# Optimization experiments

Measured on AMD Instinct MI355X. Metric: run time of the kernel, lower is better.

Reference implementation:

```python
import jax, jax.numpy as jnp
import numpy as np

N = 768          # nodes
E_HALF = 12288   # undirected edges (both directions added -> E = 24576)
P = 4096         # query pairs
H = 32           # hidden_dim_1wl == hidden_dim_2wl
MAX_X = 100
EPS = 1e-5
LAYER1 = 2


def setup_inputs() -> dict:
    key = jax.random.key(0)
    ks = jax.random.split(key, 12)
    s = 0.1
    x = jax.random.randint(ks[0], (N,), 0, MAX_X + 1)
    half = jax.random.randint(ks[1], (2, E_HALF), 0, N)
    ei = jnp.concatenate([half, half[::-1]], axis=1)          # symmetric edge set [2,E]
    pos = jax.random.randint(ks[2], (P, 2), 0, N)
    emb = jax.random.normal(ks[3], (MAX_X + 1, H)) * s
    gcn_W = jax.random.normal(ks[4], (LAYER1, H, H)) * s
    gcn_b = jnp.zeros((LAYER1, H))
    mlp1_W = jax.random.normal(ks[5], (2 * H, H)) * s
    mlp1_b = jnp.zeros((H,))
    mlp2_W = jax.random.normal(ks[6], (2 * H, H)) * s
    mlp2_b = jnp.zeros((H,))
    mlp3_W = jax.random.normal(ks[7], (H + 1, H)) * s
    mlp3_b = jnp.zeros((H,))
    lin_W = jax.random.normal(ks[8], (2 * H, 1)) * s
    lin_b = jnp.zeros((1,))
    return dict(x=x, ei=ei, pos=pos, emb=emb, gcn_W=gcn_W, gcn_b=gcn_b,
                mlp1_W=mlp1_W, mlp1_b=mlp1_b, mlp2_W=mlp2_W, mlp2_b=mlp2_b,
                mlp3_W=mlp3_W, mlp3_b=mlp3_b, lin_W=lin_W, lin_b=lin_b)


def _graph_norm(h):
    # PyG-style GraphNorm with default params (mean_scale=1, weight=1, bias=0)
    h = h - h.mean(0)
    return h * jax.lax.rsqrt((h * h).mean(0) + EPS)


def reference(x, ei, pos, emb, gcn_W, gcn_b, mlp1_W, mlp1_b,
              mlp2_W, mlp2_b, mlp3_W, mlp3_b, lin_W, lin_b):
    n = x.shape[0]
    d = emb.shape[1]
    h = emb[x]                                                 # [n,H] (dropout=0)
    # --- GCNConv stack: Ahat = D^-1/2 (A+I) D^-1/2 ---
    A = jnp.zeros((n, n), h.dtype).at[ei[0], ei[1]].set(1.0)
    Ahat = A + jnp.eye(n, dtype=h.dtype)
    dinv = jax.lax.rsqrt(Ahat.sum(1))
    An = Ahat * dinv[:, None] * dinv[None, :]
    for l in range(gcn_W.shape[0]):
        h = An @ (h @ gcn_W[l]) + gcn_b[l]
        h = jax.nn.relu(_graph_norm(h))                        # GraphNorm + ReLU
    # --- pair features ---
    xx = h[pos[:, 0]] * h[pos[:, 1]]                           # [P,H]
    val = jnp.concatenate([h[ei[0]], h[ei[1]]], 1)             # [E,2H]
    xe = jax.nn.relu(val @ mlp1_W + mlp1_b)                    # mlps_1
    mul = jax.nn.relu(val @ mlp2_W + mlp2_b)                   # mlps_2[0]
    # --- sparse_bmm as dense [n,n,d] contraction (coalesce sums duplicates -> .add) ---
    Xd = jnp.zeros((n, n, d), h.dtype).at[ei[0], ei[1]].add(xe)
    Md = jnp.zeros((n, n, d), h.dtype).at[ei[0], ei[1]].add(mul)
    C = jnp.einsum('ikd,kjd->ijd', Xd, Md)                     # x_{ij} = sum_k x_{ik}*mul_{kj}
    # support of the sparse result: 2-hop pairs union original edges (sparse_cat)
    adj_b = jnp.zeros((n, n), bool).at[ei[0], ei[1]].set(True)
    af = adj_b.astype(h.dtype)
    mask = ((af @ af) > 0) | adj_b
    ind = af[..., None]                                        # ones-column for original edges
    value = jnp.concatenate([C, ind], -1)                      # [n,n,H+1]
    z = value @ mlp3_W + mlp3_b                                # mlps_3[0]
    # GraphNorm over the edge support only (faithful to sparse values())
    m = mask.astype(h.dtype)[..., None]
    cnt = m.sum()
    mean = (z * m).sum((0, 1)) / cnt
    z = z - mean
    var = ((z * z) * m).sum((0, 1)) / cnt
    z = jax.nn.relu(z * jax.lax.rsqrt(var + EPS))
    # x * sm: multiply by transposed values; zero outside support (= add_zero)
    sym = z * jnp.swapaxes(z, 0, 1) * m
    pair = sym[pos[:, 0], pos[:, 1]]                           # [P,H] (edge_list gather)
    out = jnp.concatenate([pair, xx], 1) @ lin_W + lin_b       # lin_dir -> [P,1]
    return out
```

## Files before the change

kernel.cpp:

```cpp
#include <hip/hip_runtime.h>
#include <hip/hip_bf16.h>

#define NN 768
#define NE 24576
#define NPOS 4096
#define NCELL (NN*NN)
#define NBLK 2304
#define NBLK2 1152
#define NREP 16

typedef __hip_bfloat16 bf16;

__device__ __forceinline__ float ldf(const void* p, int i, int mode) {
    return mode ? __bfloat162float(((const bf16*)p)[i]) : ((const float*)p)[i];
}
__device__ __forceinline__ float aread(float* p) { return atomicAdd(p, 0.f); }
__device__ __forceinline__ int areadi(int* p) { return atomicAdd(p, 0); }

template<int D, int HALF>
__device__ __forceinline__ void redRound(float* v, int lane) {
#pragma unroll
    for (int i = 0; i < HALF; i++) {
        float snd = (lane & D) ? v[i] : v[i + HALF];
        float r = __shfl_xor(snd, D);
        v[i] = ((lane & D) ? v[i + HALF] : v[i]) + r;
    }
}

#define DOT4(Z, A, W) Z += A.x * W.x + A.y * W.y + A.z * W.z + A.w * W.w

#define GATH(rec, q0,q1,q2,q3,q4,q5,q6,q7) { \
    const float4* xr = xep4 + (rec).x * 8; \
    const float4* mr = mulp4 + (rec).y * 8; \
    float4 xv0 = xr[0], xv1 = xr[1], xv2 = xr[2], xv3 = xr[3]; \
    float4 xv4 = xr[4], xv5 = xr[5], xv6 = xr[6], xv7 = xr[7]; \
    float4 mv0 = mr[0], mv1 = mr[1], mv2 = mr[2], mv3 = mr[3]; \
    float4 mv4 = mr[4], mv5 = mr[5], mv6 = mr[6], mv7 = mr[7]; \
    q0.x += xv0.x*mv0.x; q0.y += xv0.y*mv0.y; q0.z += xv0.z*mv0.z; q0.w += xv0.w*mv0.w; \
    q1.x += xv1.x*mv1.x; q1.y += xv1.y*mv1.y; q1.z += xv1.z*mv1.z; q1.w += xv1.w*mv1.w; \
    q2.x += xv2.x*mv2.x; q2.y += xv2.y*mv2.y; q2.z += xv2.z*mv2.z; q2.w += xv2.w*mv2.w; \
    q3.x += xv3.x*mv3.x; q3.y += xv3.y*mv3.y; q3.z += xv3.z*mv3.z; q3.w += xv3.w*mv3.w; \
    q4.x += xv4.x*mv4.x; q4.y += xv4.y*mv4.y; q4.z += xv4.z*mv4.z; q4.w += xv4.w*mv4.w; \
    q5.x += xv5.x*mv5.x; q5.y += xv5.y*mv5.y; q5.z += xv5.z*mv5.z; q5.w += xv5.w*mv5.w; \
    q6.x += xv6.x*mv6.x; q6.y += xv6.y*mv6.y; q6.z += xv6.z*mv6.z; q6.w += xv6.w*mv6.w; \
    q7.x += xv7.x*mv7.x; q7.y += xv7.y*mv7.y; q7.z += xv7.z*mv7.z; q7.w += xv7.w*mv7.w; }

__global__ void k_scatter(const int* __restrict__ ei, int* __restrict__ cell, int* __restrict__ rowlen,
                          int* __restrict__ row_ptr, float* __restrict__ dinv, int* __restrict__ dc,
                          const void* __restrict__ gW, const void* __restrict__ gB,
                          const void* __restrict__ m1W, const void* __restrict__ m1B,
                          const void* __restrict__ m2W, const void* __restrict__ m2B,
                          const void* __restrict__ m3W, const void* __restrict__ m3B,
                          const void* __restrict__ lW,  const void* __restrict__ lB,
                          const void* __restrict__ emb, int* __restrict__ modeg,
                          float* __restrict__ gwf, float* __restrict__ gbf,
                          float* __restrict__ w1f, float* __restrict__ b1f,
                          float* __restrict__ w2f, float* __restrict__ b2f,
                          float* __restrict__ w3q, float* __restrict__ linf, float* __restrict__ linb) {
    int t = threadIdx.x;
    if (blockIdx.x == 96) {
        __shared__ int bad;
        if (t == 0) bad = 0;
        __syncthreads();
        int local = 0;
        for (int i = t; i < 3232; i += 256) {
            float a = fabsf(__bfloat162float(((const bf16*)emb)[i]));
            if (!(a < 100.f)) local = 1;
        }
        if (local) atomicOr(&bad, 1);
        __syncthreads();
        int mode = bad ? 0 : 1;
        if (t == 0) *modeg = mode;
        for (int i = t; i < 2048; i += 256) {
            gwf[i] = ldf(gW, i, mode);
            w1f[i] = ldf(m1W, i, mode);
            w2f[i] = ldf(m2W, i, mode);
        }
        for (int i = t; i < 64; i += 256) { gbf[i] = ldf(gB, i, mode); linf[i] = ldf(lW, i, mode); }
        if (t < 32) { b1f[t] = ldf(m1B, t, mode); b2f[t] = ldf(m2B, t, mode); }
        for (int i = t; i < 1056; i += 256) { int c = i >> 5, d = i & 31; w3q[d * 36 + c] = ldf(m3W, i, mode); }
        if (t < 32) { w3q[t * 36 + 33] = ldf(m3B, t, mode); w3q[t * 36 + 34] = 0.f; w3q[t * 36 + 35] = 0.f; }
        if (t == 0) linb[0] = ldf(lB, 0, mode);
        return;
    }
    __shared__ int amlast;
    __shared__ int sI[256];
    int e = blockIdx.x * 256 + t;
    int a = ei[e], b = ei[NE + e];
    if ((unsigned)a < (unsigned)NN && (unsigned)b < (unsigned)NN) {
        int old = atomicAdd(&cell[a * NN + b], 1);
        if (old == 0) atomicAdd(&rowlen[a], 1);
    }
    __syncthreads();
    if (t == 0) { __threadfence(); amlast = (atomicAdd(dc, 1) == 95) ? 1 : 0; }
    __syncthreads();
    if (!amlast) return;
    int i0 = 3 * t;
    int r0 = areadi(&rowlen[i0]), r1 = areadi(&rowlen[i0 + 1]), r2 = areadi(&rowlen[i0 + 2]);
    dinv[i0]     = rsqrtf((float)r0 + 1.f);
    dinv[i0 + 1] = rsqrtf((float)r1 + 1.f);
    dinv[i0 + 2] = rsqrtf((float)r2 + 1.f);
    int s3 = r0 + r1 + r2;
    sI[t] = s3;
    __syncthreads();
    for (int off = 1; off < 256; off <<= 1) {
        int tmp = (t >= off) ? sI[t - off] : 0;
        __syncthreads();
        sI[t] += tmp;
        __syncthreads();
    }
    int excl = sI[t] - s3;
    row_ptr[i0] = excl;
    row_ptr[i0 + 1] = excl + r0;
    row_ptr[i0 + 2] = excl + r0 + r1;
    if (t == 255) row_ptr[NN] = sI[255];
}

__global__ void k_fill(int* __restrict__ cell, const int* __restrict__ row_ptr, int* __restrict__ cursor,
                       int* __restrict__ col_idx, float* __restrict__ cntv, int* __restrict__ pr_row,
                       const int* __restrict__ rowlen, int* __restrict__ rtot,
                       const int* __restrict__ x, const void* __restrict__ emb,
                       const int* __restrict__ modep, float* __restrict__ bufA) {
    int t = threadIdx.x;
    int b = blockIdx.x;
    if (b < NBLK) {
        int idx = b * 256 + t;
        int i = idx / NN;
        int j = idx - i * NN;
        int cv = cell[idx];
        if (cv > 0) {
            int p = row_ptr[i] + atomicAdd(&cursor[i], 1);
            col_idx[p] = j; cntv[p] = (float)cv; pr_row[p] = i;
            cell[idx] = p;
            atomicAdd(&rtot[i], rowlen[j]);
        } else cell[idx] = -1;
    } else {
        int idx = (b - NBLK) * 256 + t;
        int i = idx >> 5, k = idx & 31;
        int xi = x[i]; if (xi < 0) xi = 0; if (xi > 100) xi = 100;
        bufA[idx] = ldf(emb, xi * 32 + k, *modep);
    }
}

__global__ void k_aggmw0(const int* __restrict__ rtot, int* __restrict__ row_base,
                         const int* __restrict__ row_ptr, const int* __restrict__ col_idx,
                         const float* __restrict__ bufA, const float* __restrict__ dinv,
                         const float* __restrict__ gwf, const float* __restrict__ gbf,
                         float* __restrict__ bufB) {
    int t = threadIdx.x;
    if (blockIdx.x == 0) {
        __shared__ int sI[256];
        int r3[3]; int s3 = 0;
#pragma unroll
        for (int q = 0; q < 3; q++) { r3[q] = rtot[3 * t + q]; s3 += r3[q]; }
        sI[t] = s3;
        __syncthreads();
        for (int off = 1; off < 256; off <<= 1) {
            int tmp = (t >= off) ? sI[t - off] : 0;
            __syncthreads();
            sI[t] += tmp;
            __syncthreads();
        }
        int run = sI[t] - s3;
        row_base[3 * t] = run;
        row_base[3 * t + 1] = run + r3[0];
        row_base[3 * t + 2] = run + r3[0] + r3[1];
        return;
    }
    __shared__ float sg[8][32];
    int li = t >> 5, k = t & 31;
    int i = (blockIdx.x - 1) * 8 + li;
    int base = row_ptr[i], len = row_ptr[i + 1] - base;
    float di = dinv[i];
    float acc = di * bufA[i * 32 + k];
    for (int e = 0; e < len; e++) {
        int c = col_idx[base + e];
        acc += dinv[c] * bufA[c * 32 + k];
    }
    sg[li][k] = di * acc;
    __syncthreads();
    int d = k;
    float s = gbf[d];
#pragma unroll
    for (int kk = 0; kk < 32; kk++) s += sg[li][kk] * gwf[kk * 32 + d];
    bufB[i * 32 + d] = s;
}

__global__ void k_hist(const int* __restrict__ row_ptr, const int* __restrict__ col_idx,
                       const int* __restrict__ row_base,
                       int* __restrict__ pcur, int2* __restrict__ paths2, int cap,
                       const float* __restrict__ bufB, float* __restrict__ nrm0) {
    int t = threadIdx.x;
    if (blockIdx.x == NN) {
        __shared__ float r1[256], r2[256];
        int dd = t & 31, g = t >> 5;
        float s = 0.f, s2 = 0.f;
        for (int r = g; r < NN; r += 8) { float v = bufB[r * 32 + dd]; s += v; s2 += v * v; }
        r1[t] = s; r2[t] = s2;
        __syncthreads();
        if (t < 32) {
            float a = 0.f, b2 = 0.f;
            for (int k = 0; k < 8; k++) { a += r1[k * 32 + t]; b2 += r2[k * 32 + t]; }
            float mean = a / (float)NN;
            float var = b2 / (float)NN - mean * mean;
            nrm0[t] = mean;
            nrm0[32 + t] = rsqrtf(fmaxf(var, 0.f) + 1e-5f);
        }
        return;
    }
    __shared__ int hist[NN];
    __shared__ int sc[256];
    int i = blockIdx.x;
    int base = row_ptr[i], len = row_ptr[i + 1] - base;
    int rb = row_base[i];
    int wave = t >> 6, lane = t & 63;
    for (int j = t; j < NN; j += 256) hist[j] = 0;
    __syncthreads();
    for (int ee = wave; ee < len; ee += 4) {
        int k = col_idx[base + ee];
        int kb = row_ptr[k], ke = row_ptr[k + 1];
        for (int e = kb + lane; e < ke; e += 64) atomicAdd(&hist[col_idx[e]], 1);
    }
    __syncthreads();
    int h0 = hist[3 * t], h1 = hist[3 * t + 1], h2 = hist[3 * t + 2];
    int s3 = h0 + h1 + h2;
    sc[t] = s3;
    __syncthreads();
    for (int off = 1; off < 256; off <<= 1) {
        int tmp = (t >= off) ? sc[t - off] : 0;
        __syncthreads();
        sc[t] += tmp;
        __syncthreads();
    }
    int excl = sc[t] - s3;
    int n0 = i * NN + 3 * t;
    pcur[n0]     = rb + excl + h0;
    pcur[n0 + 1] = rb + excl + h0 + h1;
    pcur[n0 + 2] = rb + excl + h0 + h1 + h2;
    hist[3 * t] = excl;
    hist[3 * t + 1] = excl + h0;
    hist[3 * t + 2] = excl + h0 + h1;
    __syncthreads();
    for (int ee = wave; ee < len; ee += 4) {
        int e1 = base + ee;
        int k = col_idx[e1];
        int kb = row_ptr[k], ke = row_ptr[k + 1];
        for (int e = kb + lane; e < ke; e += 64) {
            int j = col_idx[e];
            int slot = rb + atomicAdd(&hist[j], 1);
            if (slot < cap) paths2[slot] = make_int2(e1, e);
        }
    }
}

__global__ void k_aggmw1(const int* __restrict__ row_ptr, const int* __restrict__ col_idx,
                         const float* __restrict__ bufB, const float* __restrict__ nrm0,
                         const float* __restrict__ dinv,
                         const float* __restrict__ gwf, const float* __restrict__ gbf,
                         float* __restrict__ bufA, float* __restrict__ stats1) {
    __shared__ float sg[8][32];
    int t = threadIdx.x;
    int li = t >> 5, k = t & 31;
    int i = blockIdx.x * 8 + li;
    float mk = nrm0[k], rk = nrm0[32 + k];
    int base = row_ptr[i], len = row_ptr[i + 1] - base;
    float di = dinv[i];
    float acc = di * fmaxf((bufB[i * 32 + k] - mk) * rk, 0.f);
    for (int e = 0; e < len; e++) {
        int c = col_idx[base + e];
        acc += dinv[c] * fmaxf((bufB[c * 32 + k] - mk) * rk, 0.f);
    }
    sg[li][k] = di * acc;
    __syncthreads();
    int d = k;
    const float* W = gwf + 1024;
    float s = gbf[32 + d];
#pragma unroll
    for (int kk = 0; kk < 32; kk++) s += sg[li][kk] * W[kk * 32 + d];
    bufA[i * 32 + d] = s;
    __syncthreads();
    sg[li][d] = s;
    __syncthreads();
    if (t < 32) {
        float ps = 0.f, ps2 = 0.f;
#pragma unroll
        for (int q = 0; q < 8; q++) { float v = sg[q][t]; ps += v; ps2 += v * v; }
        float* rep = stats1 + (blockIdx.x & (NREP - 1)) * 80;
        atomicAdd(&rep[t], ps);
        atomicAdd(&rep[32 + t], ps2);
    }
}

__global__ void k_emlp(const float* __restrict__ bufA, const float* __restrict__ stats1,
                       const int* __restrict__ row_ptr, const int* __restrict__ col_idx,
                       const int* __restrict__ pr_row, const float* __restrict__ cntv,
                       const float* __restrict__ w1f, const float* __restrict__ b1f,
                       const float* __restrict__ w2f, const float* __restrict__ b2f,
                       float* __restrict__ xep, float* __restrict__ mulp, float* __restrict__ h) {
    __shared__ float nmean[32], nrstd[32];
    int t = threadIdx.x;
    int b = blockIdx.x;
    if (t < 32) {
        float s = 0.f, s2 = 0.f;
#pragma unroll
        for (int r = 0; r < NREP; r++) { s += stats1[r * 80 + t]; s2 += stats1[r * 80 + 32 + t]; }
        float mean = s / (float)NN;
        float var = s2 / (float)NN - mean * mean;
        nmean[t] = mean;
        nrstd[t] = rsqrtf(fmaxf(var, 0.f) + 1e-5f);
    }
    __syncthreads();
    if (b < 3072) {
        int d = t & 31;
        int p = b * 8 + (t >> 5);
        if (p >= row_ptr[NN]) {
            if (p < NE) { xep[p * 32 + d] = 0.f; mulp[p * 32 + d] = 0.f; }
            return;
        }
        int i = pr_row[p], j = col_idx[p];
        float a1 = b1f[d], a2 = b2f[d];
#pragma unroll
        for (int c = 0; c < 32; c++) {
            float hv = fmaxf((bufA[i * 32 + c] - nmean[c]) * nrstd[c], 0.f);
            a1 += hv * w1f[c * 32 + d];
            a2 += hv * w2f[c * 32 + d];
        }
#pragma unroll
        for (int c = 0; c < 32; c++) {
            float hv = fmaxf((bufA[j * 32 + c] - nmean[c]) * nrstd[c], 0.f);
            a1 += hv * w1f[(32 + c) * 32 + d];
            a2 += hv * w2f[(32 + c) * 32 + d];
        }
        float cv = cntv[p];
        xep[p * 32 + d]  = cv * fmaxf(a1, 0.f);
        mulp[p * 32 + d] = cv * fmaxf(a2, 0.f);
    } else {
        int idx = (b - 3072) * 256 + t;
        int d = idx & 31;
        h[idx] = fmaxf((bufA[idx] - nmean[d]) * nrstd[d], 0.f);
    }
}

__global__ __launch_bounds__(256, 2) void k_big(const int* __restrict__ pcur,
                                                const int2* __restrict__ paths2,
                                                const int* __restrict__ cell,
                                                const float4* __restrict__ xep4, const float4* __restrict__ mulp4,
                                                const float* __restrict__ w3q,
                                                float* __restrict__ stats, int* __restrict__ done,
                                                float* __restrict__ nrm, int cap) {
    __shared__ float sS1[32], sS2[32];
    __shared__ float sCm;
    __shared__ int amlast;
    int t = threadIdx.x, lane = t & 63;
    int b = blockIdx.x;
    int n0 = b * 512 + 2 * t;
    if (t == 0) sCm = 0.f;
    if (t < 32) { sS1[t] = 0.f; sS2[t] = 0.f; }
    __syncthreads();
    int p0a = (n0 == 0) ? 0 : pcur[n0 - 1];
    int p1a = pcur[n0];
    int p1b = pcur[n0 + 1];
    if (p0a > cap) p0a = cap; if (p1a > cap) p1a = cap; if (p1b > cap) p1b = cap;
    int lenA = p1a - p0a, lenB = p1b - p1a;
    int lim = (lenA > lenB) ? lenA : lenB;
    float4 a0 = {0.f,0.f,0.f,0.f}, a1 = a0, a2 = a0, a3 = a0, a4 = a0, a5 = a0, a6 = a0, a7 = a0;
    float4 c0 = a0, c1 = a0, c2 = a0, c3 = a0, c4 = a0, c5 = a0, c6 = a0, c7 = a0;
    for (int q = 0; q < lim; q++) {
        int2 recA, recB;
        bool doA = q < lenA, doB = q < lenB;
        if (doA) recA = paths2[p0a + q];
        if (doB) recB = paths2[p1a + q];
        if (doA) GATH(recA, a0, a1, a2, a3, a4, a5, a6, a7);
        if (doB) GATH(recB, c0, c1, c2, c3, c4, c5, c6, c7);
    }
    bool adja = cell[n0] >= 0;
    bool adjb = cell[n0 + 1] >= 0;
    float afa = adja ? 1.f : 0.f;
    float afb = adjb ? 1.f : 0.f;
    float mska = (lenA > 0 || adja) ? 1.f : 0.f;
    float mskb = (lenB > 0 || adjb) ? 1.f : 0.f;
#pragma unroll
    for (int ch = 0; ch < 2; ch++) {
        float v[32];
#pragma unroll
        for (int j = 0; j < 16; j++) {
            int dd = ch * 16 + j;
            const float4* wr = (const float4*)(w3q + dd * 36);
            float4 wv = wr[8];
            float za = wv.y + afa * wv.x;
            float zb = wv.y + afb * wv.x;
            wv = wr[0]; DOT4(za, a0, wv); DOT4(zb, c0, wv);
            wv = wr[1]; DOT4(za, a1, wv); DOT4(zb, c1, wv);
            wv = wr[2]; DOT4(za, a2, wv); DOT4(zb, c2, wv);
            wv = wr[3]; DOT4(za, a3, wv); DOT4(zb, c3, wv);
            wv = wr[4]; DOT4(za, a4, wv); DOT4(zb, c4, wv);
            wv = wr[5]; DOT4(za, a5, wv); DOT4(zb, c5, wv);
            wv = wr[6]; DOT4(za, a6, wv); DOT4(zb, c6, wv);
            wv = wr[7]; DOT4(za, a7, wv); DOT4(zb, c7, wv);
            v[j] = mska * za + mskb * zb;
            v[16 + j] = mska * za * za + mskb * zb * zb;
        }
#pragma unroll
        for (int i2 = 0; i2 < 32; i2++) v[i2] += __shfl_xor(v[i2], 32);
        redRound<16, 16>(v, lane);
        redRound<8, 8>(v, lane);
        redRound<4, 4>(v, lane);
        redRound<2, 2>(v, lane);
        redRound<1, 1>(v, lane);
        if (lane < 32) {
            if (lane < 16) atomicAdd(&sS1[ch * 16 + lane], v[0]);
            else           atomicAdd(&sS2[ch * 16 + lane - 16], v[0]);
        }
    }
    {
        float cm2 = mska + mskb;
        for (int off = 32; off >= 1; off >>= 1) cm2 += __shfl_xor(cm2, off);
        if (lane == 0) atomicAdd(&sCm, cm2);
    }
    __syncthreads();
    float* srep = stats + (b & (NREP - 1)) * 80;
    if (t < 32) {
        atomicAdd(&srep[t], sS1[t]);
        atomicAdd(&srep[32 + t], sS2[t]);
    }
    if (t == 32) atomicAdd(&srep[64], sCm);
    __syncthreads();
    if (t == 0) {
        __threadfence();
        amlast = (atomicAdd(done, 1) == NBLK2 - 1) ? 1 : 0;
    }
    __syncthreads();
    if (amlast && t < 32) {
        float sum1 = 0.f, sum2 = 0.f;
        for (int r = 0; r < NREP; r++) {
            sum1 += aread(&stats[r * 80 + t]);
            sum2 += aread(&stats[r * 80 + 32 + t]);
        }
        float cmv = 0.f;
        for (int r = 0; r < NREP; r++) cmv += aread(&stats[r * 80 + 64]);
        if (cmv < 1.f) cmv = 1.f;
        float mean = sum1 / cmv;
        float var = sum2 / cmv - mean * mean;
        nrm[t] = mean;
        nrm[32 + t] = rsqrtf(fmaxf(var, 0.f) + 1e-5f);
    }
}

__global__ void k_out(const int* __restrict__ pos, const int* __restrict__ pcur,
                      const int2* __restrict__ paths2,
                      const int* __restrict__ cell,
                      const float* __restrict__ xep, const float* __restrict__ mulp,
                      const float* __restrict__ h,
                      const float* __restrict__ w3q,
                      const float* __restrict__ nrm,
                      const float* __restrict__ linf, const float* __restrict__ linb,
                      const int* __restrict__ modep, int cap, void* __restrict__ outp) {
    __shared__ float Cb[4][2][32];
    int t = threadIdx.x;
    int w = t >> 6, lane = t & 63, d = lane & 31, dir = lane >> 5;
    int p = blockIdx.x * 4 + w;
    int a = pos[2 * p], b = pos[2 * p + 1];
    if ((unsigned)a >= (unsigned)NN) a = 0;
    if ((unsigned)b >= (unsigned)NN) b = 0;
    int r = dir ? b : a;
    int cc = dir ? a : b;
    int n = r * NN + cc;
    int p1 = pcur[n];
    int p0 = (n == 0) ? 0 : pcur[n - 1];
    if (p0 > cap) p0 = cap; if (p1 > cap) p1 = cap;
    float acc = 0.f;
    for (int q = p0; q < p1; q++) {
        int2 rec = paths2[q];
        acc += xep[rec.x * 32 + d] * mulp[rec.y * 32 + d];
    }
    Cb[w][dir][d] = acc;
    bool adj = cell[n] >= 0;
    float msk = (p1 > p0 || adj) ? 1.f : 0.f;
    __syncthreads();
    float z = w3q[d * 36 + 33] + (adj ? 1.f : 0.f) * w3q[d * 36 + 32];
#pragma unroll
    for (int c = 0; c < 32; c++) z += Cb[w][dir][c] * w3q[d * 36 + c];
    float zn = fmaxf((z - nrm[d]) * nrm[32 + d], 0.f);
    float zp = __shfl_xor(zn, 32);
    float symd = msk * zn * zp;
    float xxd = h[a * 32 + d] * h[b * 32 + d];
    float contrib = symd * linf[d] + xxd * linf[32 + d];
    for (int off = 16; off >= 1; off >>= 1) contrib += __shfl_xor(contrib, off);
    if (lane == 0) {
        float v = contrib + linb[0];
        v = fminf(fmaxf(v, -1e4f), 1e4f);
        if (*modep) ((bf16*)outp)[p] = __float2bfloat16(v);
        else        ((float*)outp)[p] = v;
    }
}

extern "C" void kernel_launch(void* const* d_in, const int* in_sizes, int n_in,
                              void* d_out, int out_size, void* d_ws, size_t ws_size,
                              hipStream_t stream) {
    const void* px  = d_in[0];  const void* pei = d_in[1];  const void* ppos = d_in[2];
    const void* pemb = d_in[3]; const void* pgW = d_in[4];  const void* pgB  = d_in[5];
    const void* pm1W = d_in[6]; const void* pm1B = d_in[7]; const void* pm2W = d_in[8];
    const void* pm2B = d_in[9]; const void* pm3W = d_in[10]; const void* pm3B = d_in[11];
    const void* plW = d_in[12]; const void* plB = d_in[13];
    {
        int c2048 = 0, c64 = 0, c32 = 0;
        for (int i = 0; i < n_in; i++) {
            int s = in_sizes[i]; const void* p = d_in[i];
            switch (s) {
                case 768:   px = p; break;
                case 49152: pei = p; break;
                case 8192:  ppos = p; break;
                case 3232:  pemb = p; break;
                case 2048:  if (c2048 == 0) pgW = p; else if (c2048 == 1) pm1W = p; else pm2W = p; c2048++; break;
                case 64:    if (c64 == 0) pgB = p; else plW = p; c64++; break;
                case 32:    if (c32 == 0) pm1B = p; else if (c32 == 1) pm2B = p; else pm3B = p; c32++; break;
                case 1056:  pm3W = p; break;
                case 1:     plB = p; break;
                default: break;
            }
        }
    }

    char* ws = (char*)d_ws;
    size_t off = 0;
    auto alloc = [&](size_t bytes) -> void* {
        void* pp = ws + off;
        off += (bytes + 255) & ~(size_t)255;
        return pp;
    };
    int*   cell    = (int*)alloc(NCELL * 4);
    int*   pcur    = (int*)alloc(NCELL * 4);
    char*  aux0    = ws + off;
    int*   rowlen  = (int*)alloc(NN * 4);
    int*   rtot    = (int*)alloc(NN * 4);
    int*   cursor  = (int*)alloc(NN * 4);
    float* stats   = (float*)alloc(NREP * 80 * 4);
    float* stats1  = (float*)alloc(NREP * 80 * 4);
    int*   dcs     = (int*)alloc(8 * 4);
    size_t auxlen  = (ws + off) - aux0;
    int*   row_base= (int*)alloc(NN * 4);
    int*   row_ptr = (int*)alloc((NN + 1) * 4);
    int*   col_idx = (int*)alloc(NE * 4);
    float* cntv    = (float*)alloc(NE * 4);
    int*   pr_row  = (int*)alloc(NE * 4);
    float* dinv    = (float*)alloc(NN * 4);
    float* h       = (float*)alloc(NN * 32 * 4);
    float* bufA    = (float*)alloc(NN * 32 * 4);
    float* bufB    = (float*)alloc(NN * 32 * 4);
    float* xep     = (float*)alloc(NE * 32 * 4);
    float* mulp    = (float*)alloc(NE * 32 * 4);
    float* nrm     = (float*)alloc(64 * 4);
    float* nrm0    = (float*)alloc(64 * 4);
    float* gwf     = (float*)alloc(2048 * 4);
    float* gbf     = (float*)alloc(64 * 4);
    float* w1f     = (float*)alloc(2048 * 4);
    float* b1f     = (float*)alloc(32 * 4);
    float* w2f     = (float*)alloc(2048 * 4);
    float* b2f     = (float*)alloc(32 * 4);
    float* w3q     = (float*)alloc(32 * 36 * 4);
    float* linf    = (float*)alloc(64 * 4);
    float* linb    = (float*)alloc(4);
    int*   modeg   = (int*)alloc(4);
    size_t remain = (ws_size > off) ? (ws_size - off) : 0;
    int cap = (int)(remain / 8);
    if (cap > (1 << 20)) cap = (1 << 20);
    int2*  paths2  = (int2*)alloc((size_t)cap * 8);

    hipMemsetAsync(cell, 0, (size_t)NCELL * 4, stream);
    hipMemsetAsync(aux0, 0, auxlen, stream);
    k_scatter<<<97, 256, 0, stream>>>((const int*)pei, cell, rowlen, row_ptr, dinv, &dcs[0],
                                      pgW, pgB, pm1W, pm1B, pm2W, pm2B, pm3W, pm3B, plW, plB,
                                      pemb, modeg, gwf, gbf, w1f, b1f, w2f, b2f, w3q, linf, linb);
    k_fill<<<NBLK + 96, 256, 0, stream>>>(cell, row_ptr, cursor, col_idx, cntv, pr_row,
                                          rowlen, rtot, (const int*)px, pemb, modeg, bufA);
    k_aggmw0<<<1 + 96, 256, 0, stream>>>(rtot, row_base, row_ptr, col_idx, bufA, dinv, gwf, gbf, bufB);
    k_hist<<<NN + 1, 256, 0, stream>>>(row_ptr, col_idx, row_base, pcur, paths2, cap, bufB, nrm0);
    k_aggmw1<<<96, 256, 0, stream>>>(row_ptr, col_idx, bufB, nrm0, dinv, gwf, gbf, bufA, stats1);
    k_emlp<<<3072 + 96, 256, 0, stream>>>(bufA, stats1, row_ptr, col_idx, pr_row, cntv,
                                          w1f, b1f, w2f, b2f, xep, mulp, h);
    k_big<<<NBLK2, 256, 0, stream>>>(pcur, paths2, cell, (const float4*)xep, (const float4*)mulp,
                                     w3q, stats, &dcs[1], nrm, cap);
    k_out<<<NPOS / 4, 256, 0, stream>>>((const int*)ppos, pcur, paths2, cell, xep, mulp, h,
                                        w3q, nrm, linf, linb, modeg, cap, d_out);
}
```

Before: 305.3 us.

## Rebalance k_big by flattening path records across threads with LDS atomics

k_big previously assigned two cells per thread, so path-list length imbalance serialized work within waves. Now each block handles 128 cells and distributes all (path, quarter) items of its contiguous range evenly over threads, accumulating into shared memory with atomics. This needs the destination cell encoded into the upper bits of the path record, with edge indices limited to 15 bits. The per-cell linear map and GraphNorm statistics are then computed from LDS with a transposed weight copy. The cost is heavy LDS atomic traffic and reliance on the 15-bit packing bound.

```diff
diff --git a/kernel.cpp b/kernel.cpp
--- a/kernel.cpp
+++ b/kernel.cpp
@@ -6,7 +6,8 @@
 #define NPOS 4096
 #define NCELL (NN*NN)
 #define NBLK 2304
-#define NBLK2 1152
+#define NBIG 4608
+#define BCELLS 128
 #define NREP 16
 
 typedef __hip_bfloat16 bf16;
@@ -16,34 +17,6 @@
 }
 __device__ __forceinline__ float aread(float* p) { return atomicAdd(p, 0.f); }
 __device__ __forceinline__ int areadi(int* p) { return atomicAdd(p, 0); }
-
-template<int D, int HALF>
-__device__ __forceinline__ void redRound(float* v, int lane) {
-#pragma unroll
-    for (int i = 0; i < HALF; i++) {
-        float snd = (lane & D) ? v[i] : v[i + HALF];
-        float r = __shfl_xor(snd, D);
-        v[i] = ((lane & D) ? v[i + HALF] : v[i]) + r;
-    }
-}
-
-#define DOT4(Z, A, W) Z += A.x * W.x + A.y * W.y + A.z * W.z + A.w * W.w
-
-#define GATH(rec, q0,q1,q2,q3,q4,q5,q6,q7) { \
-    const float4* xr = xep4 + (rec).x * 8; \
-    const float4* mr = mulp4 + (rec).y * 8; \
-    float4 xv0 = xr[0], xv1 = xr[1], xv2 = xr[2], xv3 = xr[3]; \
-    float4 xv4 = xr[4], xv5 = xr[5], xv6 = xr[6], xv7 = xr[7]; \
-    float4 mv0 = mr[0], mv1 = mr[1], mv2 = mr[2], mv3 = mr[3]; \
-    float4 mv4 = mr[4], mv5 = mr[5], mv6 = mr[6], mv7 = mr[7]; \
-    q0.x += xv0.x*mv0.x; q0.y += xv0.y*mv0.y; q0.z += xv0.z*mv0.z; q0.w += xv0.w*mv0.w; \
-    q1.x += xv1.x*mv1.x; q1.y += xv1.y*mv1.y; q1.z += xv1.z*mv1.z; q1.w += xv1.w*mv1.w; \
-    q2.x += xv2.x*mv2.x; q2.y += xv2.y*mv2.y; q2.z += xv2.z*mv2.z; q2.w += xv2.w*mv2.w; \
-    q3.x += xv3.x*mv3.x; q3.y += xv3.y*mv3.y; q3.z += xv3.z*mv3.z; q3.w += xv3.w*mv3.w; \
-    q4.x += xv4.x*mv4.x; q4.y += xv4.y*mv4.y; q4.z += xv4.z*mv4.z; q4.w += xv4.w*mv4.w; \
-    q5.x += xv5.x*mv5.x; q5.y += xv5.y*mv5.y; q5.z += xv5.z*mv5.z; q5.w += xv5.w*mv5.w; \
-    q6.x += xv6.x*mv6.x; q6.y += xv6.y*mv6.y; q6.z += xv6.z*mv6.z; q6.w += xv6.w*mv6.w; \
-    q7.x += xv7.x*mv7.x; q7.y += xv7.y*mv7.y; q7.z += xv7.z*mv7.z; q7.w += xv7.w*mv7.w; }
 
 __global__ void k_scatter(const int* __restrict__ ei, int* __restrict__ cell, int* __restrict__ rowlen,
                           int* __restrict__ row_ptr, float* __restrict__ dinv, int* __restrict__ dc,
@@ -248,7 +221,11 @@
         for (int e = kb + lane; e < ke; e += 64) {
             int j = col_idx[e];
             int slot = rb + atomicAdd(&hist[j], 1);
-            if (slot < cap) paths2[slot] = make_int2(e1, e);
+            if (slot < cap) {
+                unsigned n2 = (unsigned)(i * NN + j);
+                paths2[slot] = make_int2((int)((unsigned)e1 | ((n2 & 0x1FFFFu) << 15)),
+                                         (int)((unsigned)e  | ((n2 >> 17) << 15)));
+            }
         }
     }
 }
@@ -341,83 +318,84 @@
     }
 }
 
-__global__ __launch_bounds__(256, 2) void k_big(const int* __restrict__ pcur,
+__global__ __launch_bounds__(256, 4) void k_big(const int* __restrict__ pcur,
                                                 const int2* __restrict__ paths2,
                                                 const int* __restrict__ cell,
                                                 const float4* __restrict__ xep4, const float4* __restrict__ mulp4,
                                                 const float* __restrict__ w3q,
                                                 float* __restrict__ stats, int* __restrict__ done,
                                                 float* __restrict__ nrm, int cap) {
+    __shared__ float Cb[BCELLS * 36];
+    __shared__ float w3t[1024];
     __shared__ float sS1[32], sS2[32];
     __shared__ float sCm;
     __shared__ int amlast;
-    int t = threadIdx.x, lane = t & 63;
+    int t = threadIdx.x;
     int b = blockIdx.x;
-    int n0 = b * 512 + 2 * t;
+    int cell0 = b * BCELLS;
+    for (int i = t; i < BCELLS * 36; i += 256) Cb[i] = 0.f;
+    for (int i = t; i < 1024; i += 256) w3t[i] = w3q[(i & 31) * 36 + (i >> 5)];
     if (t == 0) sCm = 0.f;
     if (t < 32) { sS1[t] = 0.f; sS2[t] = 0.f; }
     __syncthreads();
-    int p0a = (n0 == 0) ? 0 : pcur[n0 - 1];
-    int p1a = pcur[n0];
-    int p1b = pcur[n0 + 1];
-    if (p0a > cap) p0a = cap; if (p1a > cap) p1a = cap; if (p1b > cap) p1b = cap;
-    int lenA = p1a - p0a, lenB = p1b - p1a;
-    int lim = (lenA > lenB) ? lenA : lenB;
-    float4 a0 = {0.f,0.f,0.f,0.f}, a1 = a0, a2 = a0, a3 = a0, a4 = a0, a5 = a0, a6 = a0, a7 = a0;
-    float4 c0 = a0, c1 = a0, c2 = a0, c3 = a0, c4 = a0, c5 = a0, c6 = a0, c7 = a0;
-    for (int q = 0; q < lim; q++) {
-        int2 recA, recB;
-        bool doA = q < lenA, doB = q < lenB;
-        if (doA) recA = paths2[p0a + q];
-        if (doB) recB = paths2[p1a + q];
-        if (doA) GATH(recA, a0, a1, a2, a3, a4, a5, a6, a7);
-        if (doB) GATH(recB, c0, c1, c2, c3, c4, c5, c6, c7);
-    }
-    bool adja = cell[n0] >= 0;
-    bool adjb = cell[n0 + 1] >= 0;
-    float afa = adja ? 1.f : 0.f;
-    float afb = adjb ? 1.f : 0.f;
-    float mska = (lenA > 0 || adja) ? 1.f : 0.f;
-    float mskb = (lenB > 0 || adjb) ? 1.f : 0.f;
-#pragma unroll
-    for (int ch = 0; ch < 2; ch++) {
-        float v[32];
-#pragma unroll
-        for (int j = 0; j < 16; j++) {
-            int dd = ch * 16 + j;
-            const float4* wr = (const float4*)(w3q + dd * 36);
-            float4 wv = wr[8];
-            float za = wv.y + afa * wv.x;
-            float zb = wv.y + afb * wv.x;
-            wv = wr[0]; DOT4(za, a0, wv); DOT4(zb, c0, wv);
-            wv = wr[1]; DOT4(za, a1, wv); DOT4(zb, c1, wv);
-            wv = wr[2]; DOT4(za, a2, wv); DOT4(zb, c2, wv);
-            wv = wr[3]; DOT4(za, a3, wv); DOT4(zb, c3, wv);
-            wv = wr[4]; DOT4(za, a4, wv); DOT4(zb, c4, wv);
-            wv = wr[5]; DOT4(za, a5, wv); DOT4(zb, c5, wv);
-            wv = wr[6]; DOT4(za, a6, wv); DOT4(zb, c6, wv);
-            wv = wr[7]; DOT4(za, a7, wv); DOT4(zb, c7, wv);
-            v[j] = mska * za + mskb * zb;
-            v[16 + j] = mska * za * za + mskb * zb * zb;
-        }
-#pragma unroll
-        for (int i2 = 0; i2 < 32; i2++) v[i2] += __shfl_xor(v[i2], 32);
-        redRound<16, 16>(v, lane);
-        redRound<8, 8>(v, lane);
-        redRound<4, 4>(v, lane);
-        redRound<2, 2>(v, lane);
-        redRound<1, 1>(v, lane);
-        if (lane < 32) {
-            if (lane < 16) atomicAdd(&sS1[ch * 16 + lane], v[0]);
-            else           atomicAdd(&sS2[ch * 16 + lane - 16], v[0]);
-        }
-    }
-    {
-        float cm2 = mska + mskb;
-        for (int off = 32; off >= 1; off >>= 1) cm2 += __shfl_xor(cm2, off);
-        if (lane == 0) atomicAdd(&sCm, cm2);
-    }
-    __syncthreads();
+
+    int pstart = (cell0 == 0) ? 0 : pcur[cell0 - 1];
+    int pend = pcur[cell0 + BCELLS - 1];
+    if (pstart > cap) pstart = cap;
+    if (pend > cap) pend = cap;
+    int nitems = (pend - pstart) * 8;
+    for (int idx = t; idx < nitems; idx += 256) {
+        int p = pstart + (idx >> 3);
+        int q = idx & 7;
+        int2 rec = paths2[p];
+        unsigned rx = (unsigned)rec.x, ry = (unsigned)rec.y;
+        int cl = (int)((rx >> 15) | ((ry >> 15) << 17)) - cell0;
+        int e1 = (int)(rx & 0x7FFFu);
+        int e2 = (int)(ry & 0x7FFFu);
+        float4 xv = xep4[e1 * 8 + q];
+        float4 mv = mulp4[e2 * 8 + q];
+        float* cp = Cb + cl * 36 + q * 4;
+        atomicAdd(cp + 0, xv.x * mv.x);
+        atomicAdd(cp + 1, xv.y * mv.y);
+        atomicAdd(cp + 2, xv.z * mv.z);
+        atomicAdd(cp + 3, xv.w * mv.w);
+    }
+    __syncthreads();
+
+    int d = t & 31, half = t >> 5, lane = t & 63;
+    float wcol[32];
+#pragma unroll
+    for (int c = 0; c < 32; c++) wcol[c] = w3t[c * 32 + d];
+    float bd  = w3q[d * 36 + 33];
+    float wid = w3q[d * 36 + 32];
+    float s1 = 0.f, s2 = 0.f, cmv = 0.f;
+    for (int pass = 0; pass < BCELLS / 8; pass++) {
+        int cl = pass * 8 + half;
+        int n = cell0 + cl;
+        int p1 = pcur[n];
+        int p0 = (n == 0) ? 0 : pcur[n - 1];
+        if (p0 > cap) p0 = cap;
+        if (p1 > cap) p1 = cap;
+        bool adj = cell[n] >= 0;
+        float msk = (p1 > p0 || adj) ? 1.f : 0.f;
+        float z = bd + (adj ? 1.f : 0.f) * wid;
+        const float4* cr = (const float4*)(Cb + cl * 36);
+#pragma unroll
+        for (int k = 0; k < 8; k++) {
+            float4 cv = cr[k];
+            z += cv.x * wcol[4 * k] + cv.y * wcol[4 * k + 1] + cv.z * wcol[4 * k + 2] + cv.w * wcol[4 * k + 3];
+        }
+        s1 += msk * z;
+        s2 += msk * z * z;
+        if (d == 0) cmv += msk;
+    }
+    s1 += __shfl_xor(s1, 32);
+    s2 += __shfl_xor(s2, 32);
+    cmv += __shfl_xor(cmv, 32);
+    if (lane < 32) { atomicAdd(&sS1[lane], s1); atomicAdd(&sS2[lane], s2); }
+    if (lane == 0) atomicAdd(&sCm, cmv);
+    __syncthreads();
+
     float* srep = stats + (b & (NREP - 1)) * 80;
     if (t < 32) {
         atomicAdd(&srep[t], sS1[t]);
@@ -427,7 +405,7 @@
     __syncthreads();
     if (t == 0) {
         __threadfence();
-        amlast = (atomicAdd(done, 1) == NBLK2 - 1) ? 1 : 0;
+        amlast = (atomicAdd(done, 1) == NBIG - 1) ? 1 : 0;
     }
     __syncthreads();
     if (amlast && t < 32) {
@@ -436,11 +414,11 @@
             sum1 += aread(&stats[r * 80 + t]);
             sum2 += aread(&stats[r * 80 + 32 + t]);
         }
-        float cmv = 0.f;
-        for (int r = 0; r < NREP; r++) cmv += aread(&stats[r * 80 + 64]);
-        if (cmv < 1.f) cmv = 1.f;
-        float mean = sum1 / cmv;
-        float var = sum2 / cmv - mean * mean;
+        float cmt = 0.f;
+        for (int r = 0; r < NREP; r++) cmt += aread(&stats[r * 80 + 64]);
+        if (cmt < 1.f) cmt = 1.f;
+        float mean = sum1 / cmt;
+        float var = sum2 / cmt - mean * mean;
         nrm[t] = mean;
         nrm[32 + t] = rsqrtf(fmaxf(var, 0.f) + 1e-5f);
     }
@@ -471,7 +449,9 @@
     float acc = 0.f;
     for (int q = p0; q < p1; q++) {
         int2 rec = paths2[q];
-        acc += xep[rec.x * 32 + d] * mulp[rec.y * 32 + d];
+        int e1 = (int)((unsigned)rec.x & 0x7FFFu);
+        int e2 = (int)((unsigned)rec.y & 0x7FFFu);
+        acc += xep[e1 * 32 + d] * mulp[e2 * 32 + d];
     }
     Cb[w][dir][d] = acc;
     bool adj = cell[n] >= 0;
@@ -578,8 +558,8 @@
     k_aggmw1<<<96, 256, 0, stream>>>(row_ptr, col_idx, bufB, nrm0, dinv, gwf, gbf, bufA, stats1);
     k_emlp<<<3072 + 96, 256, 0, stream>>>(bufA, stats1, row_ptr, col_idx, pr_row, cntv,
                                           w1f, b1f, w2f, b2f, xep, mulp, h);
-    k_big<<<NBLK2, 256, 0, stream>>>(pcur, paths2, cell, (const float4*)xep, (const float4*)mulp,
-                                     w3q, stats, &dcs[1], nrm, cap);
+    k_big<<<NBIG, 256, 0, stream>>>(pcur, paths2, cell, (const float4*)xep, (const float4*)mulp,
+                                    w3q, stats, &dcs[1], nrm, cap);
     k_out<<<NPOS / 4, 256, 0, stream>>>((const int*)ppos, pcur, paths2, cell, xep, mulp, h,
                                         w3q, nrm, linf, linb, modeg, cap, d_out);
 }
```

Measured after the change: 404.7 us. +32.6%, slower.

## Parallelize k_big path gathers across wave lanes with shared-memory cell staging

Applied to the files above, without the earlier changes.

Before, each thread in k_big owned two cells and serially gathered full 32-wide xep/mulp rows per 2-hop path, so work was imbalanced and each thread held many float4 registers. Now each wave walks 64 cells one at a time. Its lanes split the path list by parity and the 32 feature channels, and the per-cell sums go into shared memory. The MLP and stats step then reads one cell per thread. The change also packs the destination cell index into the high bits of the paths2 records, which k_out masks off. It adds shared-memory traffic, a shuffle loop, and twice as many blocks in exchange for coalesced gathers and better load balance.

```diff
diff --git a/kernel.cpp b/kernel.cpp
--- a/kernel.cpp
+++ b/kernel.cpp
@@ -6,7 +6,8 @@
 #define NPOS 4096
 #define NCELL (NN*NN)
 #define NBLK 2304
-#define NBLK2 1152
+#define NBIG 2304
+#define BCELLS 256
 #define NREP 16
 
 typedef __hip_bfloat16 bf16;
@@ -28,22 +29,6 @@
 }
 
 #define DOT4(Z, A, W) Z += A.x * W.x + A.y * W.y + A.z * W.z + A.w * W.w
-
-#define GATH(rec, q0,q1,q2,q3,q4,q5,q6,q7) { \
-    const float4* xr = xep4 + (rec).x * 8; \
-    const float4* mr = mulp4 + (rec).y * 8; \
-    float4 xv0 = xr[0], xv1 = xr[1], xv2 = xr[2], xv3 = xr[3]; \
-    float4 xv4 = xr[4], xv5 = xr[5], xv6 = xr[6], xv7 = xr[7]; \
-    float4 mv0 = mr[0], mv1 = mr[1], mv2 = mr[2], mv3 = mr[3]; \
-    float4 mv4 = mr[4], mv5 = mr[5], mv6 = mr[6], mv7 = mr[7]; \
-    q0.x += xv0.x*mv0.x; q0.y += xv0.y*mv0.y; q0.z += xv0.z*mv0.z; q0.w += xv0.w*mv0.w; \
-    q1.x += xv1.x*mv1.x; q1.y += xv1.y*mv1.y; q1.z += xv1.z*mv1.z; q1.w += xv1.w*mv1.w; \
-    q2.x += xv2.x*mv2.x; q2.y += xv2.y*mv2.y; q2.z += xv2.z*mv2.z; q2.w += xv2.w*mv2.w; \
-    q3.x += xv3.x*mv3.x; q3.y += xv3.y*mv3.y; q3.z += xv3.z*mv3.z; q3.w += xv3.w*mv3.w; \
-    q4.x += xv4.x*mv4.x; q4.y += xv4.y*mv4.y; q4.z += xv4.z*mv4.z; q4.w += xv4.w*mv4.w; \
-    q5.x += xv5.x*mv5.x; q5.y += xv5.y*mv5.y; q5.z += xv5.z*mv5.z; q5.w += xv5.w*mv5.w; \
-    q6.x += xv6.x*mv6.x; q6.y += xv6.y*mv6.y; q6.z += xv6.z*mv6.z; q6.w += xv6.w*mv6.w; \
-    q7.x += xv7.x*mv7.x; q7.y += xv7.y*mv7.y; q7.z += xv7.z*mv7.z; q7.w += xv7.w*mv7.w; }
 
 __global__ void k_scatter(const int* __restrict__ ei, int* __restrict__ cell, int* __restrict__ rowlen,
                           int* __restrict__ row_ptr, float* __restrict__ dinv, int* __restrict__ dc,
@@ -248,7 +233,11 @@
         for (int e = kb + lane; e < ke; e += 64) {
             int j = col_idx[e];
             int slot = rb + atomicAdd(&hist[j], 1);
-            if (slot < cap) paths2[slot] = make_int2(e1, e);
+            if (slot < cap) {
+                unsigned n2 = (unsigned)(i * NN + j);
+                paths2[slot] = make_int2((int)((unsigned)e1 | ((n2 & 0x1FFFFu) << 15)),
+                                         (int)((unsigned)e  | ((n2 >> 17) << 15)));
+            }
         }
     }
 }
@@ -341,44 +330,58 @@
     }
 }
 
-__global__ __launch_bounds__(256, 2) void k_big(const int* __restrict__ pcur,
+__global__ __launch_bounds__(256, 4) void k_big(const int* __restrict__ pcur,
                                                 const int2* __restrict__ paths2,
-                                                const int* __restrict__ cell,
-                                                const float4* __restrict__ xep4, const float4* __restrict__ mulp4,
+                                                const int* __restrict__ cellA,
+                                                const float* __restrict__ xep, const float* __restrict__ mulp,
                                                 const float* __restrict__ w3q,
                                                 float* __restrict__ stats, int* __restrict__ done,
                                                 float* __restrict__ nrm, int cap) {
+    __shared__ float Cb[BCELLS * 36];
     __shared__ float sS1[32], sS2[32];
     __shared__ float sCm;
     __shared__ int amlast;
-    int t = threadIdx.x, lane = t & 63;
+    int t = threadIdx.x;
     int b = blockIdx.x;
-    int n0 = b * 512 + 2 * t;
+    int cell0 = b * BCELLS;
+    for (int i = t; i < BCELLS * 9; i += 256) ((float4*)Cb)[i] = make_float4(0.f, 0.f, 0.f, 0.f);
     if (t == 0) sCm = 0.f;
     if (t < 32) { sS1[t] = 0.f; sS2[t] = 0.f; }
     __syncthreads();
-    int p0a = (n0 == 0) ? 0 : pcur[n0 - 1];
-    int p1a = pcur[n0];
-    int p1b = pcur[n0 + 1];
-    if (p0a > cap) p0a = cap; if (p1a > cap) p1a = cap; if (p1b > cap) p1b = cap;
-    int lenA = p1a - p0a, lenB = p1b - p1a;
-    int lim = (lenA > lenB) ? lenA : lenB;
-    float4 a0 = {0.f,0.f,0.f,0.f}, a1 = a0, a2 = a0, a3 = a0, a4 = a0, a5 = a0, a6 = a0, a7 = a0;
-    float4 c0 = a0, c1 = a0, c2 = a0, c3 = a0, c4 = a0, c5 = a0, c6 = a0, c7 = a0;
-    for (int q = 0; q < lim; q++) {
-        int2 recA, recB;
-        bool doA = q < lenA, doB = q < lenB;
-        if (doA) recA = paths2[p0a + q];
-        if (doB) recB = paths2[p1a + q];
-        if (doA) GATH(recA, a0, a1, a2, a3, a4, a5, a6, a7);
-        if (doB) GATH(recB, c0, c1, c2, c3, c4, c5, c6, c7);
-    }
-    bool adja = cell[n0] >= 0;
-    bool adjb = cell[n0 + 1] >= 0;
-    float afa = adja ? 1.f : 0.f;
-    float afb = adjb ? 1.f : 0.f;
-    float mska = (lenA > 0 || adja) ? 1.f : 0.f;
-    float mskb = (lenB > 0 || adjb) ? 1.f : 0.f;
+
+    int wid = t >> 6, lane = t & 63, half = lane >> 5, d = lane & 31;
+    int myn = cell0 + wid + 4 * lane;
+    int p1v = pcur[myn];
+    int p0v = (myn == 0) ? 0 : pcur[myn - 1];
+    int adjv = cellA[myn];
+    if (p0v > cap) p0v = cap;
+    if (p1v > cap) p1v = cap;
+    for (int it = 0; it < 64; it++) {
+        int p1 = __shfl(p1v, it);
+        int p0 = __shfl(p0v, it);
+        int adj = __shfl(adjv, it);
+        int ncl = wid + 4 * it;
+        int P = p1 - p0;
+        if (P <= 0) {
+            if (adj >= 0 && lane < 2) Cb[ncl * 36 + 32 + lane] = 1.f;
+            continue;
+        }
+        float acc = 0.f;
+        for (int q = half; q < P; q += 2) {
+            int2 rec = paths2[p0 + q];
+            int e1 = rec.x & 0x7FFF, e2 = rec.y & 0x7FFF;
+            acc += xep[e1 * 32 + d] * mulp[e2 * 32 + d];
+        }
+        acc += __shfl_xor(acc, 32);
+        if (lane < 32) Cb[ncl * 36 + lane] = acc;
+        else if (lane < 34) Cb[ncl * 36 + lane] = (lane == 32) ? (adj >= 0 ? 1.f : 0.f) : 1.f;
+    }
+    __syncthreads();
+
+    const float4* cr = (const float4*)(Cb + t * 36);
+    float4 c0 = cr[0], c1 = cr[1], c2 = cr[2], c3 = cr[3];
+    float4 c4 = cr[4], c5 = cr[5], c6 = cr[6], c7 = cr[7];
+    float af = Cb[t * 36 + 32], msk = Cb[t * 36 + 33];
 #pragma unroll
     for (int ch = 0; ch < 2; ch++) {
         float v[32];
@@ -387,18 +390,17 @@
             int dd = ch * 16 + j;
             const float4* wr = (const float4*)(w3q + dd * 36);
             float4 wv = wr[8];
-            float za = wv.y + afa * wv.x;
-            float zb = wv.y + afb * wv.x;
-            wv = wr[0]; DOT4(za, a0, wv); DOT4(zb, c0, wv);
-            wv = wr[1]; DOT4(za, a1, wv); DOT4(zb, c1, wv);
-            wv = wr[2]; DOT4(za, a2, wv); DOT4(zb, c2, wv);
-            wv = wr[3]; DOT4(za, a3, wv); DOT4(zb, c3, wv);
-            wv = wr[4]; DOT4(za, a4, wv); DOT4(zb, c4, wv);
-            wv = wr[5]; DOT4(za, a5, wv); DOT4(zb, c5, wv);
-            wv = wr[6]; DOT4(za, a6, wv); DOT4(zb, c6, wv);
-            wv = wr[7]; DOT4(za, a7, wv); DOT4(zb, c7, wv);
-            v[j] = mska * za + mskb * zb;
-            v[16 + j] = mska * za * za + mskb * zb * zb;
+            float za = wv.y + af * wv.x;
+            wv = wr[0]; DOT4(za, c0, wv);
+            wv = wr[1]; DOT4(za, c1, wv);
+            wv = wr[2]; DOT4(za, c2, wv);
+            wv = wr[3]; DOT4(za, c3, wv);
+            wv = wr[4]; DOT4(za, c4, wv);
+            wv = wr[5]; DOT4(za, c5, wv);
+            wv = wr[6]; DOT4(za, c6, wv);
+            wv = wr[7]; DOT4(za, c7, wv);
+            v[j] = msk * za;
+            v[16 + j] = msk * za * za;
         }
 #pragma unroll
         for (int i2 = 0; i2 < 32; i2++) v[i2] += __shfl_xor(v[i2], 32);
@@ -413,7 +415,7 @@
         }
     }
     {
-        float cm2 = mska + mskb;
+        float cm2 = msk;
         for (int off = 32; off >= 1; off >>= 1) cm2 += __shfl_xor(cm2, off);
         if (lane == 0) atomicAdd(&sCm, cm2);
     }
@@ -427,7 +429,7 @@
     __syncthreads();
     if (t == 0) {
         __threadfence();
-        amlast = (atomicAdd(done, 1) == NBLK2 - 1) ? 1 : 0;
+        amlast = (atomicAdd(done, 1) == NBIG - 1) ? 1 : 0;
     }
     __syncthreads();
     if (amlast && t < 32) {
@@ -436,11 +438,11 @@
             sum1 += aread(&stats[r * 80 + t]);
             sum2 += aread(&stats[r * 80 + 32 + t]);
         }
-        float cmv = 0.f;
-        for (int r = 0; r < NREP; r++) cmv += aread(&stats[r * 80 + 64]);
-        if (cmv < 1.f) cmv = 1.f;
-        float mean = sum1 / cmv;
-        float var = sum2 / cmv - mean * mean;
+        float cmt = 0.f;
+        for (int r = 0; r < NREP; r++) cmt += aread(&stats[r * 80 + 64]);
+        if (cmt < 1.f) cmt = 1.f;
+        float mean = sum1 / cmt;
+        float var = sum2 / cmt - mean * mean;
         nrm[t] = mean;
         nrm[32 + t] = rsqrtf(fmaxf(var, 0.f) + 1e-5f);
     }
@@ -471,7 +473,9 @@
     float acc = 0.f;
     for (int q = p0; q < p1; q++) {
         int2 rec = paths2[q];
-        acc += xep[rec.x * 32 + d] * mulp[rec.y * 32 + d];
+        int e1 = (int)((unsigned)rec.x & 0x7FFFu);
+        int e2 = (int)((unsigned)rec.y & 0x7FFFu);
+        acc += xep[e1 * 32 + d] * mulp[e2 * 32 + d];
     }
     Cb[w][dir][d] = acc;
     bool adj = cell[n] >= 0;
@@ -578,8 +582,8 @@
     k_aggmw1<<<96, 256, 0, stream>>>(row_ptr, col_idx, bufB, nrm0, dinv, gwf, gbf, bufA, stats1);
     k_emlp<<<3072 + 96, 256, 0, stream>>>(bufA, stats1, row_ptr, col_idx, pr_row, cntv,
                                           w1f, b1f, w2f, b2f, xep, mulp, h);
-    k_big<<<NBLK2, 256, 0, stream>>>(pcur, paths2, cell, (const float4*)xep, (const float4*)mulp,
-                                     w3q, stats, &dcs[1], nrm, cap);
+    k_big<<<NBIG, 256, 0, stream>>>(pcur, paths2, cell, xep, mulp,
+                                    w3q, stats, &dcs[1], nrm, cap);
     k_out<<<NPOS / 4, 256, 0, stream>>>((const int*)ppos, pcur, paths2, cell, xep, mulp, h,
                                         w3q, nrm, linf, linb, modeg, cap, d_out);
 }
```

Measured after the change: 382.9 us. 25.4% more time.
